# Optimization experiments

Measured on AMD Instinct MI355X. Metric: run time of the kernel, lower is better.

Reference implementation:

```python
import jax, jax.numpy as jnp
import numpy as np

N_NODES = 50000

def _gcn_conv(x, W, b, src, dst, num_nodes):
    # PyG GCNConv: linear transform, then D^{-1/2} A_hat D^{-1/2} aggregation (A_hat has self-loops).
    xw = x @ W                                   # [N, out]
    ones = jnp.ones(src.shape[0], dtype=x.dtype)
    deg = jax.ops.segment_sum(ones, dst, num_segments=num_nodes)  # in-degree incl. self loop
    dinv = jnp.where(deg > 0, jax.lax.rsqrt(deg), 0.0)
    norm = dinv[src] * dinv[dst]                 # [E]
    msg = xw[src] * norm[:, None]                # [E, out] gather + scale
    out = jax.ops.segment_sum(msg, dst, num_segments=num_nodes)   # scatter-add
    return out + b

def _add_self_loops(edge_index, num_nodes):
    loop = jnp.arange(num_nodes, dtype=edge_index.dtype)
    src = jnp.concatenate([edge_index[0], loop])
    dst = jnp.concatenate([edge_index[1], loop])
    return src, dst

def setup_inputs() -> dict:
    key = jax.random.key(0)
    k = jax.random.split(key, 6)
    in_dim, hid_dim, out_dim = 256, 128, 64
    n_edges = 800000
    x = jax.random.normal(k[0], (N_NODES, in_dim), dtype=jnp.float32)
    edge_index = jax.random.randint(k[1], (2, n_edges), 0, N_NODES, dtype=jnp.int64)
    W1 = jax.random.normal(k[2], (in_dim, hid_dim), dtype=jnp.float32) / np.sqrt(in_dim)
    b1 = jnp.zeros((hid_dim,), dtype=jnp.float32)
    W2 = jax.random.normal(k[3], (hid_dim, out_dim), dtype=jnp.float32) / np.sqrt(hid_dim)
    b2 = jnp.zeros((out_dim,), dtype=jnp.float32)
    return {"x": x, "edge_index": edge_index, "W1": W1, "b1": b1, "W2": W2, "b2": b2}

def reference(x, edge_index, W1, b1, W2, b2):
    src, dst = _add_self_loops(edge_index, N_NODES)
    h = jnp.tanh(_gcn_conv(x, W1, b1, src, dst, N_NODES))
    out = _gcn_conv(h, W2, b2, src, dst, N_NODES)
    return out
```

## Files before the change

### kernel.cpp

```cpp
#include <hip/hip_runtime.h>

#define INDIM 256
#define HID 128
#define OUTD 64
#define BINSHIFT 8
#define MAXBIN 256

typedef _Float16 f16x8 __attribute__((ext_vector_type(8)));
typedef float    f32x4 __attribute__((ext_vector_type(4)));

__global__ __launch_bounds__(256) void k_hist_setup(const int* __restrict__ dst, int* __restrict__ bin_counts,
                                                    int E,
                                                    const float* __restrict__ W1, const float* __restrict__ W2,
                                                    _Float16* __restrict__ W1t, _Float16* __restrict__ W2t) {
    __shared__ int h[MAXBIN];
    int tid = threadIdx.x;
    h[tid] = 0;
    __syncthreads();
    int base = blockIdx.x * 4096;
#pragma unroll
    for (int i = 0; i < 16; i++) {
        int e = base + i * 256 + tid;
        if (e < E) atomicAdd(&h[dst[e] >> BINSHIFT], 1);
    }
    __syncthreads();
    int v = h[tid];
    if (v) atomicAdd(&bin_counts[tid], v);

    constexpr int NW1 = HID * INDIM;
    constexpr int NW2 = OUTD * HID;
    int id = blockIdx.x * 256 + tid;
    if (id < NW1) {
        int n = id / INDIM, k = id % INDIM;
        W1t[id] = (_Float16)W1[k * HID + n];
    } else if (id < NW1 + NW2) {
        int j = id - NW1;
        int n = j / HID, k = j % HID;
        W2t[j] = (_Float16)W2[k * OUTD + n];
    }
}

__global__ __launch_bounds__(256) void k_bscan(const int* __restrict__ bin_counts,
                                               int* __restrict__ bin_start, int* __restrict__ bin_cursor,
                                               int* __restrict__ row_start, int NBIN, int M, int E) {
    __shared__ int s[256];
    int tid = threadIdx.x;
    int v = (tid < NBIN) ? bin_counts[tid] : 0;
    s[tid] = v;
    __syncthreads();
#pragma unroll
    for (int off = 1; off < 256; off <<= 1) {
        int t = (tid >= off) ? s[tid - off] : 0;
        __syncthreads();
        s[tid] += t;
        __syncthreads();
    }
    if (tid < NBIN) {
        int excl = s[tid] - v;
        bin_start[tid] = excl;
        bin_cursor[tid] = excl;
    }
    if (tid == 0) {
        bin_start[NBIN] = E;
        row_start[M] = E;
    }
}

__global__ __launch_bounds__(256) void k_binfill(const int* __restrict__ src, const int* __restrict__ dst,
                                                 int* __restrict__ bin_cursor, int* __restrict__ binned, int E) {
    __shared__ int h[MAXBIN];
    __shared__ int rb[MAXBIN];
    int tid = threadIdx.x;
    h[tid] = 0;
    __syncthreads();
    int base = blockIdx.x * 2048;
    int ep[8], eb[8], rk[8];
#pragma unroll
    for (int i = 0; i < 8; i++) {
        int e = base + i * 256 + tid;
        if (e < E) {
            int s = src[e], d = dst[e];
            ep[i] = (s << 8) | (d & 255);
            eb[i] = d >> BINSHIFT;
            rk[i] = atomicAdd(&h[eb[i]], 1);
        } else {
            eb[i] = -1;
        }
    }
    __syncthreads();
    int c = h[tid];
    if (c) rb[tid] = atomicAdd(&bin_cursor[tid], c);
    __syncthreads();
#pragma unroll
    for (int i = 0; i < 8; i++) {
        if (eb[i] >= 0) binned[rb[eb[i]] + rk[i]] = ep[i];
    }
}

__global__ __launch_bounds__(256) void k_csr(const int* __restrict__ binned, const int* __restrict__ bin_start,
                                             int* __restrict__ row_start, float* __restrict__ dinv,
                                             int* __restrict__ edge_src, int M) {
    __shared__ int cnt[256];
    __shared__ int s[256];
    __shared__ int cur[256];
    int b = blockIdx.x, tid = threadIdx.x;
    int beg = bin_start[b], end = bin_start[b + 1];
    cnt[tid] = 0;
    __syncthreads();
    for (int i = beg + tid; i < end; i += 256) {
        atomicAdd(&cnt[binned[i] & 255], 1);
    }
    __syncthreads();
    int c = cnt[tid];
    s[tid] = c;
    __syncthreads();
#pragma unroll
    for (int off = 1; off < 256; off <<= 1) {
        int t = (tid >= off) ? s[tid - off] : 0;
        __syncthreads();
        s[tid] += t;
        __syncthreads();
    }
    int start = beg + s[tid] - c;
    int node = (b << BINSHIFT) + tid;
    if (node < M) {
        row_start[node] = start;
        dinv[node] = rsqrtf(1.0f + (float)c);
    }
    cur[tid] = start;
    __syncthreads();
    for (int i = beg + tid; i < end; i += 256) {
        int p = binned[i];
        int pos = atomicAdd(&cur[p & 255], 1);
        edge_src[pos] = p >> 8;
    }
}

template <int BN, int K, typename AT>
__global__ __launch_bounds__(256) void k_gemm_mfma(
    const AT* __restrict__ X, const _Float16* __restrict__ Wt,
    const float* __restrict__ dinv, _Float16* __restrict__ XW16, int M)
{
    constexpr int BM = 64;
    constexpr int BK = 32;
    constexpr int NT = BN / 16;
    constexpr int LDK = BK + 8;

    __shared__ __align__(16) _Float16 As[BM][LDK];
    __shared__ __align__(16) _Float16 Bs[BN][LDK];

    const int tid  = threadIdx.x;
    const int wave = tid >> 6;
    const int lane = tid & 63;
    const int m    = lane & 15;
    const int q    = lane >> 4;
    const int rb   = blockIdx.x * BM;

    f32x4 acc[NT];
#pragma unroll
    for (int t = 0; t < NT; t++) acc[t] = (f32x4){0.f, 0.f, 0.f, 0.f};

    for (int kt = 0; kt < K; kt += BK) {
        if (kt) __syncthreads();
        if constexpr (sizeof(AT) == 4) {
#pragma unroll
            for (int i = 0; i < BM * 8 / 256; i++) {
                int ch  = tid + i * 256;
                int row = ch >> 3;
                int c4  = ch & 7;
                int gr  = rb + row;
                float4 v = make_float4(0.f, 0.f, 0.f, 0.f);
                if (gr < M) v = *(const float4*)((const float*)X + (long)gr * K + kt + c4 * 4);
                _Float16* p = &As[row][c4 * 4];
                p[0] = (_Float16)v.x; p[1] = (_Float16)v.y;
                p[2] = (_Float16)v.z; p[3] = (_Float16)v.w;
            }
        } else {
            int row = tid >> 2;
            int c8  = tid & 3;
            int gr  = rb + row;
            uint4 v = make_uint4(0u, 0u, 0u, 0u);
            if (gr < M) v = *(const uint4*)((const _Float16*)X + (long)gr * K + kt + c8 * 8);
            *(uint4*)(&As[row][c8 * 8]) = v;
        }
#pragma unroll
        for (int i = 0; i < BN * 8 / 256; i++) {
            int ch = tid + i * 256;
            int n  = ch >> 3;
            int c4 = ch & 7;
            *(ushort4*)(&Bs[n][c4 * 4]) =
                *(const ushort4*)(Wt + (long)n * K + kt + c4 * 4);
        }
        __syncthreads();

        f16x8 af = *(const f16x8*)(&As[wave * 16 + m][q * 8]);
#pragma unroll
        for (int t = 0; t < NT; t++) {
            f16x8 bf = *(const f16x8*)(&Bs[t * 16 + m][q * 8]);
            acc[t] = __builtin_amdgcn_mfma_f32_16x16x32_f16(af, bf, acc[t], 0, 0, 0);
        }
    }

    int row0 = rb + wave * 16 + q * 4;
#pragma unroll
    for (int r = 0; r < 4; r++) {
        int row = row0 + r;
        if (row < M) {
            float di = dinv[row];
#pragma unroll
            for (int t = 0; t < NT; t++) {
                XW16[(long)row * BN + t * 16 + m] = (_Float16)(acc[t][r] * di);
            }
        }
    }
}

template <int F, bool TANH, typename OutT>
__global__ __launch_bounds__(256) void k_agg_csr(const int* __restrict__ row_start,
                                                 const int* __restrict__ edge_src,
                                                 const _Float16* __restrict__ feat,
                                                 const float* __restrict__ bias,
                                                 const float* __restrict__ dinv,
                                                 OutT* __restrict__ out, int M) {
    constexpr int LPN = F / 8;
    constexpr int NPB = 256 / LPN;
    int n = blockIdx.x * NPB + threadIdx.x / LPN;
    int c = threadIdx.x % LPN;
    if (n >= M) return;
    int beg = row_start[n], end = row_start[n + 1];

    f16x8 self = *(const f16x8*)(feat + (long)n * F + c * 8);
    float acc[8], acc2[8];
#pragma unroll
    for (int k = 0; k < 8; k++) { acc[k] = (float)self[k]; acc2[k] = 0.f; }

    int j = beg;
    for (; j + 3 < end; j += 4) {
        int s0 = edge_src[j],     s1 = edge_src[j + 1];
        int s2 = edge_src[j + 2], s3 = edge_src[j + 3];
        f16x8 v0 = *(const f16x8*)(feat + (long)s0 * F + c * 8);
        f16x8 v1 = *(const f16x8*)(feat + (long)s1 * F + c * 8);
        f16x8 v2 = *(const f16x8*)(feat + (long)s2 * F + c * 8);
        f16x8 v3 = *(const f16x8*)(feat + (long)s3 * F + c * 8);
#pragma unroll
        for (int k = 0; k < 8; k++) {
            acc[k]  += (float)v0[k] + (float)v1[k];
            acc2[k] += (float)v2[k] + (float)v3[k];
        }
    }
    for (; j < end; j++) {
        int s = edge_src[j];
        f16x8 v = *(const f16x8*)(feat + (long)s * F + c * 8);
#pragma unroll
        for (int k = 0; k < 8; k++) acc[k] += (float)v[k];
    }

    float di = dinv[n];
#pragma unroll
    for (int k = 0; k < 8; k++) acc[k] = bias[c * 8 + k] + di * (acc[k] + acc2[k]);
    if (TANH) {
#pragma unroll
        for (int k = 0; k < 8; k++) acc[k] = tanhf(acc[k]);
    }
    if constexpr (sizeof(OutT) == 2) {
        f16x8 o;
#pragma unroll
        for (int k = 0; k < 8; k++) o[k] = (_Float16)acc[k];
        __builtin_nontemporal_store(o, (f16x8*)((_Float16*)out + (long)n * F + c * 8));
    } else {
        f32x4 o0 = {acc[0], acc[1], acc[2], acc[3]};
        f32x4 o1 = {acc[4], acc[5], acc[6], acc[7]};
        float* p = (float*)out + (long)n * F + c * 8;
        __builtin_nontemporal_store(o0, (f32x4*)p);
        __builtin_nontemporal_store(o1, (f32x4*)(p + 4));
    }
}

extern "C" void kernel_launch(void* const* d_in, const int* in_sizes, int n_in,
                              void* d_out, int out_size, void* d_ws, size_t ws_size,
                              hipStream_t stream) {
    const float* x  = (const float*)d_in[0];
    const int*   ei = (const int*)d_in[1];
    const float* W1 = (const float*)d_in[2];
    const float* b1 = (const float*)d_in[3];
    const float* W2 = (const float*)d_in[4];
    const float* b2 = (const float*)d_in[5];
    float* out = (float*)d_out;

    const int M = in_sizes[0] / INDIM;
    const int E = in_sizes[1] / 2;
    const int* srcp = ei;
    const int* dstp = ei + E;

    const int Mp   = (M + 63) & ~63;
    const int NBIN = (M + 255) >> BINSHIFT;

    float*     dinv       = (float*)d_ws;
    int*       row_start  = (int*)(dinv + Mp);
    int*       bin_start  = row_start + Mp;
    int*       bin_cursor = bin_start + 258;
    int*       bin_counts = bin_cursor + MAXBIN;
    _Float16*  W1t        = (_Float16*)(bin_counts + MAXBIN);
    _Float16*  W2t        = W1t + HID * INDIM;
    int*       binned     = (int*)(W2t + OUTD * HID);
    int*       edge_src   = binned + E;
    _Float16*  xw16       = (_Float16*)(edge_src + E);
    _Float16*  h16        = xw16 + (long)M * HID;
    _Float16*  hw16       = xw16;

    const int NWH = (E + 4095) / 4096;
    const int NWF = (E + 2047) / 2048;

    hipMemsetAsync(bin_counts, 0, MAXBIN * sizeof(int), stream);
    k_hist_setup<<<NWH, 256, 0, stream>>>(dstp, bin_counts, E, W1, W2, W1t, W2t);
    k_bscan<<<1, 256, 0, stream>>>(bin_counts, bin_start, bin_cursor, row_start, NBIN, M, E);
    k_binfill<<<NWF, 256, 0, stream>>>(srcp, dstp, bin_cursor, binned, E);
    k_csr<<<NBIN, 256, 0, stream>>>(binned, bin_start, row_start, dinv, edge_src, M);

    k_gemm_mfma<HID, INDIM, float><<<(M + 63) / 64, 256, 0, stream>>>(x, W1t, dinv, xw16, M);
    k_agg_csr<HID, true, _Float16><<<(M + 15) / 16, 256, 0, stream>>>(row_start, edge_src, xw16, b1, dinv, h16, M);

    k_gemm_mfma<OUTD, HID, _Float16><<<(M + 63) / 64, 256, 0, stream>>>(h16, W2t, dinv, hw16, M);
    k_agg_csr<OUTD, false, float><<<(M + 31) / 32, 256, 0, stream>>>(row_start, edge_src, hw16, b2, dinv, out, M);
}
```

Baseline: 228.2 us.

## Co-schedule first GEMM with CSR build stages and move source normalization into aggregation

The separate scan kernel is removed. Each bin-fill and CSR block now recomputes the bin prefix scan locally. The first-layer GEMM is split across the bin-fill and CSR kernels as extra blocks, so its tiles overlap with the graph construction. Because the GEMM can then run before dinv exists, the source-side dinv scaling moves into the aggregation loop as a per-edge gather and FMA, and the aggregation loop is unrolled to 8. The GEMM tile grows to 128 rows with wider loads, at the cost of redundant scans, extra dinv gathers per edge, and larger shared-memory unions.

```diff
diff --git a/kernel.cpp b/kernel.cpp
--- a/kernel.cpp
+++ b/kernel.cpp
@@ -40,135 +40,37 @@
     }
 }
 
-__global__ __launch_bounds__(256) void k_bscan(const int* __restrict__ bin_counts,
-                                               int* __restrict__ bin_start, int* __restrict__ bin_cursor,
-                                               int* __restrict__ row_start, int NBIN, int M, int E) {
-    __shared__ int s[256];
-    int tid = threadIdx.x;
-    int v = (tid < NBIN) ? bin_counts[tid] : 0;
-    s[tid] = v;
-    __syncthreads();
-#pragma unroll
-    for (int off = 1; off < 256; off <<= 1) {
-        int t = (tid >= off) ? s[tid - off] : 0;
-        __syncthreads();
-        s[tid] += t;
-        __syncthreads();
-    }
-    if (tid < NBIN) {
-        int excl = s[tid] - v;
-        bin_start[tid] = excl;
-        bin_cursor[tid] = excl;
-    }
-    if (tid == 0) {
-        bin_start[NBIN] = E;
-        row_start[M] = E;
-    }
-}
-
-__global__ __launch_bounds__(256) void k_binfill(const int* __restrict__ src, const int* __restrict__ dst,
-                                                 int* __restrict__ bin_cursor, int* __restrict__ binned, int E) {
-    __shared__ int h[MAXBIN];
-    __shared__ int rb[MAXBIN];
-    int tid = threadIdx.x;
-    h[tid] = 0;
-    __syncthreads();
-    int base = blockIdx.x * 2048;
-    int ep[8], eb[8], rk[8];
-#pragma unroll
-    for (int i = 0; i < 8; i++) {
-        int e = base + i * 256 + tid;
-        if (e < E) {
-            int s = src[e], d = dst[e];
-            ep[i] = (s << 8) | (d & 255);
-            eb[i] = d >> BINSHIFT;
-            rk[i] = atomicAdd(&h[eb[i]], 1);
-        } else {
-            eb[i] = -1;
-        }
-    }
-    __syncthreads();
-    int c = h[tid];
-    if (c) rb[tid] = atomicAdd(&bin_cursor[tid], c);
-    __syncthreads();
-#pragma unroll
-    for (int i = 0; i < 8; i++) {
-        if (eb[i] >= 0) binned[rb[eb[i]] + rk[i]] = ep[i];
-    }
-}
-
-__global__ __launch_bounds__(256) void k_csr(const int* __restrict__ binned, const int* __restrict__ bin_start,
-                                             int* __restrict__ row_start, float* __restrict__ dinv,
-                                             int* __restrict__ edge_src, int M) {
-    __shared__ int cnt[256];
-    __shared__ int s[256];
-    __shared__ int cur[256];
-    int b = blockIdx.x, tid = threadIdx.x;
-    int beg = bin_start[b], end = bin_start[b + 1];
-    cnt[tid] = 0;
-    __syncthreads();
-    for (int i = beg + tid; i < end; i += 256) {
-        atomicAdd(&cnt[binned[i] & 255], 1);
-    }
-    __syncthreads();
-    int c = cnt[tid];
-    s[tid] = c;
-    __syncthreads();
-#pragma unroll
-    for (int off = 1; off < 256; off <<= 1) {
-        int t = (tid >= off) ? s[tid - off] : 0;
-        __syncthreads();
-        s[tid] += t;
-        __syncthreads();
-    }
-    int start = beg + s[tid] - c;
-    int node = (b << BINSHIFT) + tid;
-    if (node < M) {
-        row_start[node] = start;
-        dinv[node] = rsqrtf(1.0f + (float)c);
-    }
-    cur[tid] = start;
-    __syncthreads();
-    for (int i = beg + tid; i < end; i += 256) {
-        int p = binned[i];
-        int pos = atomicAdd(&cur[p & 255], 1);
-        edge_src[pos] = p >> 8;
-    }
-}
+struct __align__(16) GemmSh { _Float16 As[128][40]; _Float16 Bs[128][40]; };
+struct FillSh { int h[256]; int s[256]; int rb[256]; };
+struct CsrSh  { int A[256]; int B[256]; int C[256]; };
+union FillU { FillSh f; GemmSh g; };
+union CsrU  { CsrSh  c; GemmSh g; };
 
 template <int BN, int K, typename AT>
-__global__ __launch_bounds__(256) void k_gemm_mfma(
-    const AT* __restrict__ X, const _Float16* __restrict__ Wt,
-    const float* __restrict__ dinv, _Float16* __restrict__ XW16, int M)
-{
-    constexpr int BM = 64;
-    constexpr int BK = 32;
+__device__ __forceinline__ void gemm_body(const AT* __restrict__ X, const _Float16* __restrict__ Wt,
+                                          _Float16* __restrict__ XW, int M, int rb,
+                                          _Float16 (*As)[40], _Float16 (*Bs)[40])
+{
     constexpr int NT = BN / 16;
-    constexpr int LDK = BK + 8;
-
-    __shared__ __align__(16) _Float16 As[BM][LDK];
-    __shared__ __align__(16) _Float16 Bs[BN][LDK];
-
     const int tid  = threadIdx.x;
     const int wave = tid >> 6;
     const int lane = tid & 63;
     const int m    = lane & 15;
     const int q    = lane >> 4;
-    const int rb   = blockIdx.x * BM;
-
-    f32x4 acc[NT];
-#pragma unroll
-    for (int t = 0; t < NT; t++) acc[t] = (f32x4){0.f, 0.f, 0.f, 0.f};
-
-    for (int kt = 0; kt < K; kt += BK) {
+
+    f32x4 acc[2][NT];
+#pragma unroll
+    for (int r = 0; r < 2; r++)
+#pragma unroll
+        for (int t = 0; t < NT; t++) acc[r][t] = (f32x4){0.f, 0.f, 0.f, 0.f};
+
+    for (int kt = 0; kt < K; kt += 32) {
         if (kt) __syncthreads();
         if constexpr (sizeof(AT) == 4) {
 #pragma unroll
-            for (int i = 0; i < BM * 8 / 256; i++) {
-                int ch  = tid + i * 256;
-                int row = ch >> 3;
-                int c4  = ch & 7;
-                int gr  = rb + row;
+            for (int i = 0; i < 4; i++) {
+                int ch = tid + i * 256;
+                int row = ch >> 3, c4 = ch & 7, gr = rb + row;
                 float4 v = make_float4(0.f, 0.f, 0.f, 0.f);
                 if (gr < M) v = *(const float4*)((const float*)X + (long)gr * K + kt + c4 * 4);
                 _Float16* p = &As[row][c4 * 4];
@@ -176,43 +78,172 @@
                 p[2] = (_Float16)v.z; p[3] = (_Float16)v.w;
             }
         } else {
-            int row = tid >> 2;
-            int c8  = tid & 3;
-            int gr  = rb + row;
-            uint4 v = make_uint4(0u, 0u, 0u, 0u);
-            if (gr < M) v = *(const uint4*)((const _Float16*)X + (long)gr * K + kt + c8 * 8);
-            *(uint4*)(&As[row][c8 * 8]) = v;
-        }
-#pragma unroll
-        for (int i = 0; i < BN * 8 / 256; i++) {
+#pragma unroll
+            for (int i = 0; i < 2; i++) {
+                int ch = tid + i * 256;
+                int row = ch >> 2, c8 = ch & 3, gr = rb + row;
+                uint4 v = make_uint4(0u, 0u, 0u, 0u);
+                if (gr < M) v = *(const uint4*)((const _Float16*)X + (long)gr * K + kt + c8 * 8);
+                *(uint4*)(&As[row][c8 * 8]) = v;
+            }
+        }
+#pragma unroll
+        for (int i = 0; i < BN / 64; i++) {
             int ch = tid + i * 256;
-            int n  = ch >> 3;
-            int c4 = ch & 7;
-            *(ushort4*)(&Bs[n][c4 * 4]) =
-                *(const ushort4*)(Wt + (long)n * K + kt + c4 * 4);
-        }
-        __syncthreads();
-
-        f16x8 af = *(const f16x8*)(&As[wave * 16 + m][q * 8]);
+            int n = ch >> 2, c8 = ch & 3;
+            *(uint4*)(&Bs[n][c8 * 8]) = *(const uint4*)(Wt + (long)n * K + kt + c8 * 8);
+        }
+        __syncthreads();
+
+        f16x8 a0 = *(const f16x8*)(&As[wave * 32 + m][q * 8]);
+        f16x8 a1 = *(const f16x8*)(&As[wave * 32 + 16 + m][q * 8]);
 #pragma unroll
         for (int t = 0; t < NT; t++) {
             f16x8 bf = *(const f16x8*)(&Bs[t * 16 + m][q * 8]);
-            acc[t] = __builtin_amdgcn_mfma_f32_16x16x32_f16(af, bf, acc[t], 0, 0, 0);
-        }
-    }
-
-    int row0 = rb + wave * 16 + q * 4;
-#pragma unroll
-    for (int r = 0; r < 4; r++) {
-        int row = row0 + r;
-        if (row < M) {
-            float di = dinv[row];
-#pragma unroll
-            for (int t = 0; t < NT; t++) {
-                XW16[(long)row * BN + t * 16 + m] = (_Float16)(acc[t][r] * di);
+            acc[0][t] = __builtin_amdgcn_mfma_f32_16x16x32_f16(a0, bf, acc[0][t], 0, 0, 0);
+            acc[1][t] = __builtin_amdgcn_mfma_f32_16x16x32_f16(a1, bf, acc[1][t], 0, 0, 0);
+        }
+    }
+
+#pragma unroll
+    for (int r2 = 0; r2 < 2; r2++) {
+        int row0 = rb + wave * 32 + r2 * 16 + q * 4;
+#pragma unroll
+        for (int rr = 0; rr < 4; rr++) {
+            int row = row0 + rr;
+            if (row < M) {
+#pragma unroll
+                for (int t = 0; t < NT; t++)
+                    XW[(long)row * BN + t * 16 + m] = (_Float16)acc[r2][t][rr];
             }
         }
     }
+}
+
+__device__ __forceinline__ void fill_body(const int* __restrict__ src, const int* __restrict__ dst,
+                                          const int* __restrict__ bin_counts, int* __restrict__ bin_cursor,
+                                          int* __restrict__ binned, int E, FillSh& sh)
+{
+    int tid = threadIdx.x;
+    sh.h[tid] = 0;
+    int v = bin_counts[tid];
+    sh.s[tid] = v;
+    __syncthreads();
+    int base = blockIdx.x * 2048;
+    int ep[8], eb[8], rk[8];
+#pragma unroll
+    for (int i = 0; i < 8; i++) {
+        int e = base + i * 256 + tid;
+        if (e < E) {
+            int s = src[e], d = dst[e];
+            ep[i] = (s << 8) | (d & 255);
+            eb[i] = d >> BINSHIFT;
+            rk[i] = atomicAdd(&sh.h[eb[i]], 1);
+        } else {
+            eb[i] = -1;
+        }
+    }
+#pragma unroll
+    for (int off = 1; off < 256; off <<= 1) {
+        int t = (tid >= off) ? sh.s[tid - off] : 0;
+        __syncthreads();
+        sh.s[tid] += t;
+        __syncthreads();
+    }
+    int c = sh.h[tid];
+    if (c) sh.rb[tid] = (sh.s[tid] - v) + atomicAdd(&bin_cursor[tid], c);
+    __syncthreads();
+#pragma unroll
+    for (int i = 0; i < 8; i++) {
+        if (eb[i] >= 0) binned[sh.rb[eb[i]] + rk[i]] = ep[i];
+    }
+}
+
+__device__ __forceinline__ void csr_body(const int* __restrict__ binned, const int* __restrict__ bin_counts,
+                                         int* __restrict__ row_start, float* __restrict__ dinv,
+                                         int* __restrict__ edge_src, int M, int E, CsrSh& sh)
+{
+    int b = blockIdx.x, tid = threadIdx.x;
+    int v = bin_counts[tid];
+    sh.A[tid] = v;
+    __syncthreads();
+#pragma unroll
+    for (int off = 1; off < 256; off <<= 1) {
+        int t = (tid >= off) ? sh.A[tid - off] : 0;
+        __syncthreads();
+        sh.A[tid] += t;
+        __syncthreads();
+    }
+    sh.B[tid] = sh.A[tid] - v;
+    __syncthreads();
+    int beg = sh.B[b];
+    int end = (b + 1 < 256) ? sh.B[b + 1] : E;
+    if (b == 0 && tid == 0) row_start[M] = E;
+
+    sh.A[tid] = 0;
+    __syncthreads();
+    for (int i = beg + tid; i < end; i += 256) {
+        atomicAdd(&sh.A[binned[i] & 255], 1);
+    }
+    __syncthreads();
+    int c = sh.A[tid];
+    sh.B[tid] = c;
+    __syncthreads();
+#pragma unroll
+    for (int off = 1; off < 256; off <<= 1) {
+        int t = (tid >= off) ? sh.B[tid - off] : 0;
+        __syncthreads();
+        sh.B[tid] += t;
+        __syncthreads();
+    }
+    int start = beg + sh.B[tid] - c;
+    int node = (b << BINSHIFT) + tid;
+    if (node < M) {
+        row_start[node] = start;
+        dinv[node] = rsqrtf(1.0f + (float)c);
+    }
+    sh.C[tid] = start;
+    __syncthreads();
+    for (int i = beg + tid; i < end; i += 256) {
+        int p = binned[i];
+        int pos = atomicAdd(&sh.C[p & 255], 1);
+        edge_src[pos] = p >> 8;
+    }
+}
+
+__global__ __launch_bounds__(256) void k_binfill_gemm(
+    const int* __restrict__ src, const int* __restrict__ dst,
+    const int* __restrict__ bin_counts, int* __restrict__ bin_cursor, int* __restrict__ binned, int E,
+    const float* __restrict__ X, const _Float16* __restrict__ W1t, _Float16* __restrict__ XW, int M,
+    int nfill, int rbofs)
+{
+    __shared__ FillU u;
+    if ((int)blockIdx.x < nfill)
+        fill_body(src, dst, bin_counts, bin_cursor, binned, E, u.f);
+    else
+        gemm_body<HID, INDIM, float>(X, W1t, XW, M, (rbofs + (int)blockIdx.x - nfill) * 128, u.g.As, u.g.Bs);
+}
+
+__global__ __launch_bounds__(256) void k_csr_gemm(
+    const int* __restrict__ binned, const int* __restrict__ bin_counts,
+    int* __restrict__ row_start, float* __restrict__ dinv, int* __restrict__ edge_src, int M, int E,
+    const float* __restrict__ X, const _Float16* __restrict__ W1t, _Float16* __restrict__ XW,
+    int nbin, int rbofs)
+{
+    __shared__ CsrU u;
+    if ((int)blockIdx.x < nbin)
+        csr_body(binned, bin_counts, row_start, dinv, edge_src, M, E, u.c);
+    else
+        gemm_body<HID, INDIM, float>(X, W1t, XW, M, (rbofs + (int)blockIdx.x - nbin) * 128, u.g.As, u.g.Bs);
+}
+
+template <int BN, int K, typename AT>
+__global__ __launch_bounds__(256) void k_gemm_mfma(const AT* __restrict__ X, const _Float16* __restrict__ Wt,
+                                                   _Float16* __restrict__ XW, int M)
+{
+    __shared__ __align__(16) _Float16 As[128][40];
+    __shared__ __align__(16) _Float16 Bs[BN][40];
+    gemm_body<BN, K, AT>(X, Wt, XW, M, (int)blockIdx.x * 128, As, Bs);
 }
 
 template <int F, bool TANH, typename OutT>
@@ -228,48 +259,80 @@
     int c = threadIdx.x % LPN;
     if (n >= M) return;
     int beg = row_start[n], end = row_start[n + 1];
+    float di = dinv[n];
 
     f16x8 self = *(const f16x8*)(feat + (long)n * F + c * 8);
     float acc[8], acc2[8];
 #pragma unroll
-    for (int k = 0; k < 8; k++) { acc[k] = (float)self[k]; acc2[k] = 0.f; }
+    for (int k = 0; k < 8; k++) { acc[k] = di * (float)self[k]; acc2[k] = 0.f; }
 
     int j = beg;
-    for (; j + 3 < end; j += 4) {
+    for (; j + 7 < end; j += 8) {
         int s0 = edge_src[j],     s1 = edge_src[j + 1];
         int s2 = edge_src[j + 2], s3 = edge_src[j + 3];
+        int s4 = edge_src[j + 4], s5 = edge_src[j + 5];
+        int s6 = edge_src[j + 6], s7 = edge_src[j + 7];
+        float d0 = dinv[s0], d1 = dinv[s1], d2 = dinv[s2], d3 = dinv[s3];
+        float d4 = dinv[s4], d5 = dinv[s5], d6 = dinv[s6], d7 = dinv[s7];
         f16x8 v0 = *(const f16x8*)(feat + (long)s0 * F + c * 8);
         f16x8 v1 = *(const f16x8*)(feat + (long)s1 * F + c * 8);
         f16x8 v2 = *(const f16x8*)(feat + (long)s2 * F + c * 8);
         f16x8 v3 = *(const f16x8*)(feat + (long)s3 * F + c * 8);
+        f16x8 v4 = *(const f16x8*)(feat + (long)s4 * F + c * 8);
+        f16x8 v5 = *(const f16x8*)(feat + (long)s5 * F + c * 8);
+        f16x8 v6 = *(const f16x8*)(feat + (long)s6 * F + c * 8);
+        f16x8 v7 = *(const f16x8*)(feat + (long)s7 * F + c * 8);
 #pragma unroll
         for (int k = 0; k < 8; k++) {
-            acc[k]  += (float)v0[k] + (float)v1[k];
-            acc2[k] += (float)v2[k] + (float)v3[k];
+            acc[k]  = fmaf(d0, (float)v0[k], acc[k]);
+            acc2[k] = fmaf(d1, (float)v1[k], acc2[k]);
+            acc[k]  = fmaf(d2, (float)v2[k], acc[k]);
+            acc2[k] = fmaf(d3, (float)v3[k], acc2[k]);
+            acc[k]  = fmaf(d4, (float)v4[k], acc[k]);
+            acc2[k] = fmaf(d5, (float)v5[k], acc2[k]);
+            acc[k]  = fmaf(d6, (float)v6[k], acc[k]);
+            acc2[k] = fmaf(d7, (float)v7[k], acc2[k]);
+        }
+    }
+    for (; j + 3 < end; j += 4) {
+        int s0 = edge_src[j],     s1 = edge_src[j + 1];
+        int s2 = edge_src[j + 2], s3 = edge_src[j + 3];
+        float d0 = dinv[s0], d1 = dinv[s1], d2 = dinv[s2], d3 = dinv[s3];
+        f16x8 v0 = *(const f16x8*)(feat + (long)s0 * F + c * 8);
+        f16x8 v1 = *(const f16x8*)(feat + (long)s1 * F + c * 8);
+        f16x8 v2 = *(const f16x8*)(feat + (long)s2 * F + c * 8);
+        f16x8 v3 = *(const f16x8*)(feat + (long)s3 * F + c * 8);
+#pragma unroll
+        for (int k = 0; k < 8; k++) {
+            acc[k]  = fmaf(d0, (float)v0[k], acc[k]);
+            acc2[k] = fmaf(d1, (float)v1[k], acc2[k]);
+            acc[k]  = fmaf(d2, (float)v2[k], acc[k]);
+            acc2[k] = fmaf(d3, (float)v3[k], acc2[k]);
         }
     }
     for (; j < end; j++) {
         int s = edge_src[j];
+        float d = dinv[s];
         f16x8 v = *(const f16x8*)(feat + (long)s * F + c * 8);
 #pragma unroll
-        for (int k = 0; k < 8; k++) acc[k] += (float)v[k];
-    }
-
-    float di = dinv[n];
-#pragma unroll
-    for (int k = 0; k < 8; k++) acc[k] = bias[c * 8 + k] + di * (acc[k] + acc2[k]);
+        for (int k = 0; k < 8; k++) acc[k] = fmaf(d, (float)v[k], acc[k]);
+    }
+
+    float r[8];
+#pragma unroll
+    for (int k = 0; k < 8; k++) r[k] = bias[c * 8 + k] + di * (acc[k] + acc2[k]);
     if (TANH) {
 #pragma unroll
-        for (int k = 0; k < 8; k++) acc[k] = tanhf(acc[k]);
+        for (int k = 0; k < 8; k++) r[k] = tanhf(r[k]);
     }
     if constexpr (sizeof(OutT) == 2) {
         f16x8 o;
 #pragma unroll
-        for (int k = 0; k < 8; k++) o[k] = (_Float16)acc[k];
+        for (int k = 0; k < 8; k++) o[k] = (_Float16)r[k];
         __builtin_nontemporal_store(o, (f16x8*)((_Float16*)out + (long)n * F + c * 8));
     } else {
-        f32x4 o0 = {acc[0], acc[1], acc[2], acc[3]};
-        f32x4 o1 = {acc[4], acc[5], acc[6], acc[7]};
+        f32x4 o0 = {r[0], r[1], r[2], r[3]};
+        f32x4 o1 = {r[4], r[5], r[6], r[7]};
         float* p = (float*)out + (long)n * F + c * 8;
         __builtin_nontemporal_store(o0, (f32x4*)p);
         __builtin_nontemporal_store(o1, (f32x4*)(p + 4));
@@ -297,8 +360,7 @@
 
     float*     dinv       = (float*)d_ws;
     int*       row_start  = (int*)(dinv + Mp);
-    int*       bin_start  = row_start + Mp;
-    int*       bin_cursor = bin_start + 258;
+    int*       bin_cursor = row_start + Mp;
     int*       bin_counts = bin_cursor + MAXBIN;
     _Float16*  W1t        = (_Float16*)(bin_counts + MAXBIN);
     _Float16*  W2t        = W1t + HID * INDIM;
@@ -310,16 +372,19 @@
 
     const int NWH = (E + 4095) / 4096;
     const int NWF = (E + 2047) / 2048;
-
-    hipMemsetAsync(bin_counts, 0, MAXBIN * sizeof(int), stream);
+    const int GB  = (M + 127) / 128;
+    const int GA  = GB / 3;
+    const int GBc = GB - GA;
+
+    hipMemsetAsync(bin_cursor, 0, 2 * MAXBIN * sizeof(int), stream);
     k_hist_setup<<<NWH, 256, 0, stream>>>(dstp, bin_counts, E, W1, W2, W1t, W2t);
-    k_bscan<<<1, 256, 0, stream>>>(bin_counts, bin_start, bin_cursor, row_start, NBIN, M, E);
-    k_binfill<<<NWF, 256, 0, stream>>>(srcp, dstp, bin_cursor, binned, E);
-    k_csr<<<NBIN, 256, 0, stream>>>(binned, bin_start, row_start, dinv, edge_src, M);
-
-    k_gemm_mfma<HID, INDIM, float><<<(M + 63) / 64, 256, 0, stream>>>(x, W1t, dinv, xw16, M);
+    k_binfill_gemm<<<NWF + GA, 256, 0, stream>>>(srcp, dstp, bin_counts, bin_cursor, binned, E,
+                                                 x, W1t, xw16, M, NWF, 0);
+    k_csr_gemm<<<NBIN + GBc, 256, 0, stream>>>(binned, bin_counts, row_start, dinv, edge_src, M, E,
+                                               x, W1t, xw16, NBIN, GA);
+
     k_agg_csr<HID, true, _Float16><<<(M + 15) / 16, 256, 0, stream>>>(row_start, edge_src, xw16, b1, dinv, h16, M);
 
-    k_gemm_mfma<OUTD, HID, _Float16><<<(M + 63) / 64, 256, 0, stream>>>(h16, W2t, dinv, hw16, M);
+    k_gemm_mfma<OUTD, HID, _Float16><<<GB, 256, 0, stream>>>(h16, W2t, hw16, M);
     k_agg_csr<OUTD, false, float><<<(M + 31) / 32, 256, 0, stream>>>(row_start, edge_src, hw16, b2, dinv, out, M);
 }
```

After: 222.0 us, median of 2. 1.03x faster.
